# Performance work log

Measured on AMD Instinct MI355X. Metric: run time of the kernel, lower is better.

## Reference

```python
import jax, jax.numpy as jnp
import numpy as np

B, D, A = 512, 32, 18          # batch, n_latent_dims (= n_heads), n_actions
FED, AED = 128, 64             # factor/action embed dims
VD = FED + AED                 # vdim = 192
KD = VD                        # kdim (key_embed_dim=None -> vdim)
HID = 256                      # per-head MLP hidden size
H = D                          # n_heads = n_latent_dims


def setup_inputs() -> dict:
    key = jax.random.key(0)
    ks = jax.random.split(key, 20)
    s = lambda i, shape: jax.random.normal(ks[i], shape, dtype=jnp.float32) * 0.05
    return {
        "features": jax.random.normal(ks[0], (B, D), dtype=jnp.float32),
        "actions": jax.random.uniform(ks[1], (B, A), dtype=jnp.float32),
        # linear projections (stored as [in, out], i.e. torch weight.T)
        "Wq": s(2, (A, KD)),  "bq": s(3, (KD,)),      # action_query_projection
        "Wk": s(4, (D, KD)),  "bk": s(5, (KD,)),      # factor_key_projection
        "Wav": s(6, (A, AED)), "bav": s(7, (AED,)),   # action_val_projection
        "Wfv": s(8, (D, FED)), "bfv": s(9, (FED,)),   # factor_val_projection
        # per-head input MLPs: vdim -> HID -> vdim (ReLU)
        "W1": s(10, (H, VD, HID)), "b1": s(11, (H, HID)),
        "W2": s(12, (H, HID, VD)), "b2": s(13, (H, VD)),
        # per-head output MLPs: vdim -> HID -> 1 (ReLU)
        "W1o": s(14, (H, VD, HID)), "b1o": s(15, (H, HID)),
        "W2o": s(16, (H, HID)),     "b2o": s(17, (H,)),
    }


def reference(features, actions, Wq, bq, Wk, bk, Wav, bav, Wfv, bfv,
              W1, b1, W2, b2, W1o, b1o, W2o, b2o):
    z, a = features, actions
    # diag_embed(z) row i = z_i * e_i, so Linear(diag_embed(z))[..., i, :] = z_i * W.T[i] + b.
    # z is expanded identically across heads, so factor embeds/keys are head-independent.
    factor_embeds = z[:, :, None] * Wfv[None] + bfv          # [B, D, FED]
    keys = z[:, :, None] * Wk[None] + bk                     # [B, D, KD]
    queries = a @ Wq + bq                                    # [B, KD]
    action_embeds = a @ Wav + bav                            # [B, AED]

    # concat factor vals with broadcast action vals -> [B, D, VD]
    cv = jnp.concatenate(
        [factor_embeds, jnp.broadcast_to(action_embeds[:, None, :], (B, D, AED))], axis=-1)

    # per-head input MLPs (ReLU), batched over heads via einsum
    h = jax.nn.relu(jnp.einsum('bdv,hvk->bhdk', cv, W1) + b1[None, :, None, :])
    values = jnp.einsum('bhdk,hkv->bhdv', h, W2) + b2[None, :, None, :]  # [B,H,D,VD]

    # attention: single query vs D keys; head-independent weights
    scores = (keys @ queries[:, :, None])[..., 0] / jnp.sqrt(jnp.float32(KD))  # [B, D]
    w = jax.nn.softmax(scores, axis=-1)                       # [B, D]
    attn_out = jnp.einsum('bd,bhdv->bhv', w, values)          # [B, H, VD]

    # per-head output MLPs (ReLU) -> scalar effect per head
    h2 = jax.nn.relu(jnp.einsum('bhv,hvk->bhk', attn_out, W1o) + b1o[None])
    effect = jnp.einsum('bhk,hk->bh', h2, W2o) + b2o[None]    # [B, H]

    attn_weights = jnp.broadcast_to(w[:, None, :], (B, H, D))  # [B, H, D]
    return effect, attn_weights
```

## Files before the change

kernel.cpp:

```cpp
#include <hip/hip_runtime.h>
#include <hip/hip_bf16.h>


typedef __attribute__((ext_vector_type(8))) short bf16x8;
typedef __attribute__((ext_vector_type(4))) short bf16x4;
typedef __attribute__((ext_vector_type(4))) float f32x4;

__device__ __forceinline__ short f2bf(float x) {
  unsigned u = __float_as_uint(x);
  u += 0x7fffu + ((u >> 16) & 1u);
  return (short)(u >> 16);
}
__device__ __forceinline__ float bf2f(unsigned short u) {
  return __uint_as_float((unsigned)u << 16);
}

__global__ __launch_bounds__(256) void kA_prep(
    const float* __restrict__ feat, const float* __restrict__ act,
    const float* __restrict__ Wq, const float* __restrict__ bq,
    const float* __restrict__ Wk,
    const float* __restrict__ Wav, const float* __restrict__ bav,
    const float* __restrict__ Wfv, const float* __restrict__ bfv,
    const float* __restrict__ W1, const float* __restrict__ b1,
    const float* __restrict__ W2, const float* __restrict__ b2,
    const float* __restrict__ W1o, const float* __restrict__ b1o,
    float* __restrict__ ws_w, float* __restrict__ ws_U,
    float* __restrict__ ws_c0, unsigned short* __restrict__ ws_Mbf,
    float* __restrict__ ws_c1, float* __restrict__ ws_W1g,
    float* __restrict__ out_aw) {
  __shared__ __align__(16) char smem[33792];
  float* sh = (float*)smem;
  const int bx = blockIdx.x;
  const int t = threadIdx.x;

  if (bx < 64) {
    const int b0 = bx * 8;
    float* sWk = sh;
    float* sA  = sh + 6144;
    float* sQk = sh + 6320;
    float* sW  = sh + 6944;
#pragma unroll
    for (int i = 0; i < 24; ++i) {
      const int idx = i * 256 + t;
      sWk[(idx % 192) * 32 + (idx / 192)] = Wk[idx];
    }
    if (t < 144) sA[t] = act[b0 * 18 + t];
    __syncthreads();
    for (int o = t; o < 608; o += 256) {
      const int j = o >> 5, d = o & 31;
      const float* arow = (j < 18) ? (Wq + j * 192) : bq;
      float acc = 0.f;
      for (int c = 0; c < 192; ++c) acc += arow[c] * sWk[c * 32 + d];
      sQk[o] = acc;
    }
    __syncthreads();
    {
      const int bi = t >> 5, d = t & 31;
      float dot = sQk[18 * 32 + d];
#pragma unroll
      for (int j = 0; j < 18; ++j) dot += sA[bi * 18 + j] * sQk[j * 32 + d];
      const float z = feat[b0 * 32 + t];
      float sc = z * dot * 0.07216878364870322f;
      float mx = sc;
#pragma unroll
      for (int off = 16; off >= 1; off >>= 1) mx = fmaxf(mx, __shfl_xor(mx, off, 64));
      const float e = __expf(sc - mx);
      float s = e;
#pragma unroll
      for (int off = 16; off >= 1; off >>= 1) s += __shfl_xor(s, off, 64);
      const float w = e / s;
      ws_w[b0 * 32 + t] = w;
      sW[t] = w;
    }
    __syncthreads();
#pragma unroll
    for (int i = 0; i < 32; ++i)
      out_aw[b0 * 1024 + i * 256 + t] = sW[(i >> 2) * 32 + (t & 31)];

  } else if (bx < 224) {
    const int r = bx - 64;
    const int h = r / 5, dt = r % 5;
    float* sF = sh;
    if (dt < 4) {
#pragma unroll
      for (int i = 0; i < 4; ++i) sF[i * 256 + t] = Wfv[dt * 1024 + i * 256 + t];
    } else {
      if (t < 128) sF[t] = bfv[t];
    }
    __syncthreads();
    if (dt < 4) {
      float acc[8];
#pragma unroll
      for (int dd = 0; dd < 8; ++dd) acc[dd] = 0.f;
#pragma unroll 4
      for (int fc = 0; fc < 32; ++fc) {
        float w1v[4];
#pragma unroll
        for (int u = 0; u < 4; ++u) w1v[u] = W1[(h * 192 + fc * 4 + u) * 256 + t];
#pragma unroll
        for (int dd = 0; dd < 8; ++dd) {
          float4 f4 = *(const float4*)(sF + dd * 128 + fc * 4);
          acc[dd] += f4.x * w1v[0] + f4.y * w1v[1] + f4.z * w1v[2] + f4.w * w1v[3];
        }
      }
#pragma unroll
      for (int dd = 0; dd < 8; ++dd)
        ws_U[(h * 32 + dt * 8 + dd) * 256 + t] = acc[dd];
    } else {
      float acc = b1[h * 256 + t];
      for (int fc = 0; fc < 32; ++fc) {
        float w1v[4];
#pragma unroll
        for (int u = 0; u < 4; ++u) w1v[u] = W1[(h * 192 + fc * 4 + u) * 256 + t];
        float4 f4 = *(const float4*)(sF + fc * 4);
        acc += f4.x * w1v[0] + f4.y * w1v[1] + f4.z * w1v[2] + f4.w * w1v[3];
      }
      for (int u = 0; u < 64; ++u)
        acc += bav[u] * W1[(h * 192 + 128 + u) * 256 + t];
      ws_c0[h * 256 + t] = acc;
    }

  } else if (bx < 480) {
    const int r = bx - 224;
    const int h = r >> 3, kt = r & 7;
    short* sW2 = (short*)smem;
    short* sB  = (short*)(smem + 13184);

    for (int i = t; i < 6144; i += 256) {
      const int row = i / 192, col = i - row * 192;
      sW2[row * 206 + col] = f2bf(W2[h * 49152 + (kt * 32 + row) * 192 + col]);
    }
    const int wv = t >> 6, lane = t & 63;
    const int quad = lane >> 4, l15 = lane & 15;

    f32x4 acc[2][4];
    const f32x4 zero = {0.f, 0.f, 0.f, 0.f};
#pragma unroll
    for (int mt = 0; mt < 2; ++mt)
#pragma unroll
      for (int nt = 0; nt < 4; ++nt) acc[mt][nt] = zero;
    float c1acc = 0.f;

    for (int kk = 0; kk < 6; ++kk) {
      __syncthreads();
#pragma unroll
      for (int vp = 0; vp < 32; vp += 2) {
        const float f0 = W1o[h * 49152 + (kk * 32 + vp) * 256 + t];
        const float f1 = W1o[h * 49152 + (kk * 32 + vp + 1) * 256 + t];
        const unsigned pack =
            ((unsigned)(unsigned short)f2bf(f1) << 16) | (unsigned short)f2bf(f0);
        *(unsigned*)(sB + t * 38 + vp) = pack;
      }
      __syncthreads();
      if (kt == 0) {
#pragma unroll
        for (int vp = 0; vp < 32; ++vp)
          c1acc += b2[h * 192 + kk * 32 + vp] * bf2f((unsigned short)sB[t * 38 + vp]);
      }
      bf16x8 a0[2];
#pragma unroll
      for (int mt = 0; mt < 2; ++mt)
        a0[mt] = *(const bf16x8*)(sW2 + (mt * 16 + l15) * 206 + kk * 32 + quad * 8);
#pragma unroll
      for (int nt = 0; nt < 4; ++nt) {
        bf16x8 b0 = *(const bf16x8*)(sB + (wv * 64 + nt * 16 + l15) * 38 + quad * 8);
#pragma unroll
        for (int mt = 0; mt < 2; ++mt)
          acc[mt][nt] = __builtin_amdgcn_mfma_f32_16x16x32_bf16(a0[mt], b0, acc[mt][nt], 0, 0, 0);
      }
    }
#pragma unroll
    for (int mt = 0; mt < 2; ++mt) {
#pragma unroll
      for (int nt = 0; nt < 4; ++nt) {
        const int col = wv * 64 + nt * 16 + l15;
        const unsigned p0 = ((unsigned)(unsigned short)f2bf(acc[mt][nt][1]) << 16) |
                            (unsigned short)f2bf(acc[mt][nt][0]);
        const unsigned p1 = ((unsigned)(unsigned short)f2bf(acc[mt][nt][3]) << 16) |
                            (unsigned short)f2bf(acc[mt][nt][2]);
        unsigned* dst = (unsigned*)(ws_Mbf + (size_t)(h * 256 + col) * 256 +
                                    kt * 32 + mt * 16 + quad * 4);
        dst[0] = p0; dst[1] = p1;
      }
    }
    if (kt == 0) ws_c1[h * 256 + t] = c1acc + b1o[h * 256 + t];

  } else {
    const int h = bx - 480;
    float accj[18];
#pragma unroll
    for (int j = 0; j < 18; ++j) accj[j] = 0.f;
#pragma unroll 4
    for (int u = 0; u < 64; ++u) {
      const float w1v = W1[(h * 192 + 128 + u) * 256 + t];
#pragma unroll
      for (int j = 0; j < 18; ++j)
        accj[j] += Wav[j * 64 + u] * w1v;
    }
#pragma unroll
    for (int j = 0; j < 18; ++j)
      ws_W1g[(h * 20 + j) * 256 + t] = accj[j];
    ws_W1g[(h * 20 + 18) * 256 + t] = 0.f;
    ws_W1g[(h * 20 + 19) * 256 + t] = 0.f;
  }
}

__global__ __launch_bounds__(256) void kB_main(
    const float* __restrict__ feat, const float* __restrict__ act,
    const float* __restrict__ ws_w, const float* __restrict__ ws_U,
    const float* __restrict__ ws_W1g, const float* __restrict__ ws_c0,
    const unsigned short* __restrict__ ws_Mbf, const float* __restrict__ ws_c1,
    const float* __restrict__ W2o, const float* __restrict__ b2o,
    float* __restrict__ out_eff) {
  const int bx = blockIdx.x;
  const int h = (bx & 7) * 4 + ((bx >> 3) & 3);
  const int bt = bx >> 5;
  const int b0 = bt * 16;
  const int t = threadIdx.x;

  __shared__ __align__(16) char smem[14208];
  short* sP   = (short*)smem;
  float* sA   = (float*)(smem + 8448);
  float* sZ   = (float*)(smem + 9728);
  float* sWw  = (float*)(smem + 11776);
  float* sRed = (float*)(smem + 13824);

  {
#pragma unroll
    for (int i = 0; i < 2; ++i) {
      sZ[i * 256 + t]  = feat[b0 * 32 + i * 256 + t];
      sWw[i * 256 + t] = ws_w[b0 * 32 + i * 256 + t];
    }
    for (int i = t; i < 320; i += 256) {
      const int row = i / 20, col = i - row * 20;
      sA[i] = (col < 18) ? act[(b0 + row) * 18 + col] : 0.f;
    }
  }
  __syncthreads();

  {
    const int bq = t >> 6, kg = t & 63;
    float g[4][4];

    {
      float4 c04 = *(const float4*)(ws_c0 + h * 256 + kg * 4);
#pragma unroll
      for (int r = 0; r < 4; ++r) {
        g[r][0] = c04.x; g[r][1] = c04.y; g[r][2] = c04.z; g[r][3] = c04.w;
      }
      const float* Wgp = ws_W1g + (h * 20) * 256 + kg * 4;
#pragma unroll
      for (int jc = 0; jc < 5; ++jc) {
        float w1q[4][4];
#pragma unroll
        for (int u = 0; u < 4; ++u) {
          float4 w4 = *(const float4*)(Wgp + (jc * 4 + u) * 256);
          w1q[u][0] = w4.x; w1q[u][1] = w4.y; w1q[u][2] = w4.z; w1q[u][3] = w4.w;
        }
        float a4[4][4];
#pragma unroll
        for (int r = 0; r < 4; ++r) {
          float4 av = *(const float4*)(sA + (bq * 4 + r) * 20 + jc * 4);
          a4[r][0] = av.x; a4[r][1] = av.y; a4[r][2] = av.z; a4[r][3] = av.w;
        }
#pragma unroll
        for (int u = 0; u < 4; ++u)
#pragma unroll
          for (int r = 0; r < 4; ++r)
#pragma unroll
            for (int c = 0; c < 4; ++c)
              g[r][c] += a4[r][u] * w1q[u][c];
      }
    }

    float acc[4][4];
#pragma unroll
    for (int r = 0; r < 4; ++r) {
      acc[r][0] = 0.f; acc[r][1] = 0.f; acc[r][2] = 0.f; acc[r][3] = 0.f;
    }
    const float* Up = ws_U + h * 8192 + kg * 4;
#pragma unroll
    for (int dc = 0; dc < 8; ++dc) {
      float uc[4][4];
#pragma unroll
      for (int dd = 0; dd < 4; ++dd) {
        float4 u4 = *(const float4*)(Up + (dc * 4 + dd) * 256);
        uc[dd][0] = u4.x; uc[dd][1] = u4.y; uc[dd][2] = u4.z; uc[dd][3] = u4.w;
      }
      float zr[4][4], wr[4][4];
#pragma unroll
      for (int r = 0; r < 4; ++r) {
        float4 z4 = *(const float4*)(sZ + (bq * 4 + r) * 32 + dc * 4);
        float4 w4 = *(const float4*)(sWw + (bq * 4 + r) * 32 + dc * 4);
        zr[r][0] = z4.x; zr[r][1] = z4.y; zr[r][2] = z4.z; zr[r][3] = z4.w;
        wr[r][0] = w4.x; wr[r][1] = w4.y; wr[r][2] = w4.z; wr[r][3] = w4.w;
      }
#pragma unroll
      for (int dd = 0; dd < 4; ++dd) {
#pragma unroll
        for (int r = 0; r < 4; ++r) {
#pragma unroll
          for (int c = 0; c < 4; ++c)
            acc[r][c] += wr[r][dd] * fmaxf(zr[r][dd] * uc[dd][c] + g[r][c], 0.f);
        }
      }
    }
#pragma unroll
    for (int r = 0; r < 4; ++r) {
      bf16x4 p;
#pragma unroll
      for (int c = 0; c < 4; ++c) p[c] = f2bf(acc[r][c]);
      *(bf16x4*)(sP + (bq * 4 + r) * 264 + kg * 4) = p;
    }
  }
  __syncthreads();

  {
    const int wv = t >> 6;
    const int lane = t & 63;
    const int quad = lane >> 4, l15 = lane & 15;

    f32x4 acc[4];
    const f32x4 zero = {0.f, 0.f, 0.f, 0.f};
#pragma unroll
    for (int nt = 0; nt < 4; ++nt) acc[nt] = zero;

    float c1r[4], w2r[4];
#pragma unroll
    for (int nt = 0; nt < 4; ++nt) {
      const int col = wv * 64 + nt * 16 + l15;
      c1r[nt] = ws_c1[h * 256 + col];
      w2r[nt] = W2o[h * 256 + col];
    }
    const unsigned short* Mp = ws_Mbf + (size_t)(h * 256 + wv * 64) * 256;

#pragma unroll
    for (int kc = 0; kc < 8; ++kc) {
      bf16x8 a0 = *(const bf16x8*)(sP + l15 * 264 + kc * 32 + quad * 8);
      bf16x8 bfr[4];
#pragma unroll
      for (int nt = 0; nt < 4; ++nt)
        bfr[nt] = *(const bf16x8*)(Mp + (nt * 16 + l15) * 256 + kc * 32 + quad * 8);
#pragma unroll
      for (int nt = 0; nt < 4; ++nt)
        acc[nt] = __builtin_amdgcn_mfma_f32_16x16x32_bf16(a0, bfr[nt], acc[nt], 0, 0, 0);
    }
#pragma unroll
    for (int r = 0; r < 4; ++r) {
      float s = fmaxf(acc[0][r] + c1r[0], 0.f) * w2r[0]
              + fmaxf(acc[1][r] + c1r[1], 0.f) * w2r[1]
              + fmaxf(acc[2][r] + c1r[2], 0.f) * w2r[2]
              + fmaxf(acc[3][r] + c1r[3], 0.f) * w2r[3];
      s += __shfl_xor(s, 1, 64);
      s += __shfl_xor(s, 2, 64);
      s += __shfl_xor(s, 4, 64);
      s += __shfl_xor(s, 8, 64);
      if (l15 == 0) sRed[(quad * 4 + r) * 4 + wv] = s;
    }
  }
  __syncthreads();
  if (t < 16) {
    float v = sRed[t * 4] + sRed[t * 4 + 1] + sRed[t * 4 + 2] + sRed[t * 4 + 3] + b2o[h];
    out_eff[(b0 + t) * 32 + h] = v;
  }
}

extern "C" void kernel_launch(void* const* d_in, const int* in_sizes, int n_in,
                              void* d_out, int out_size, void* d_ws, size_t ws_size,
                              hipStream_t stream) {
  const float* feat = (const float*)d_in[0];
  const float* act  = (const float*)d_in[1];
  const float* Wq   = (const float*)d_in[2];
  const float* bq   = (const float*)d_in[3];
  const float* Wk   = (const float*)d_in[4];
  const float* Wav  = (const float*)d_in[6];
  const float* bav  = (const float*)d_in[7];
  const float* Wfv  = (const float*)d_in[8];
  const float* bfv  = (const float*)d_in[9];
  const float* W1   = (const float*)d_in[10];
  const float* b1   = (const float*)d_in[11];
  const float* W2   = (const float*)d_in[12];
  const float* b2   = (const float*)d_in[13];
  const float* W1o  = (const float*)d_in[14];
  const float* b1o  = (const float*)d_in[15];
  const float* W2o  = (const float*)d_in[16];
  const float* b2o  = (const float*)d_in[17];
  float* out = (float*)d_out;
  float* ws = (float*)d_ws;

  float* ws_w  = ws;
  float* ws_U  = ws + 16384;
  float* ws_c0 = ws + 278528;
  float* ws_c1 = ws + 286720;
  unsigned short* ws_Mbf = (unsigned short*)(ws + 294912);
  float* ws_W1g = ws + 1343488;

  hipLaunchKernelGGL(kA_prep, dim3(512), dim3(256), 0, stream,
                     feat, act, Wq, bq, Wk, Wav, bav, Wfv, bfv, W1, b1,
                     W2, b2, W1o, b1o, ws_w, ws_U, ws_c0, ws_Mbf, ws_c1,
                     ws_W1g, out + 16384);
  hipLaunchKernelGGL(kB_main, dim3(1024), dim3(256), 0, stream,
                     feat, act, ws_w, ws_U, ws_W1g, ws_c0, ws_Mbf, ws_c1,
                     W2o, b2o, out);
}
```

Before: 146.3 us.

## Process 32 batch rows per block in kB_main with 2x2 MFMA tiles

Doubles the batch tile per block in the main kernel from 16 to 32 rows and raises the block to 512 threads across 8 waves. Each wave now covers 32 output columns for two 16-row M tiles instead of 64 columns for one. This is meant to halve the number of times the per-head bf16 M matrix and the other per-head constants are read from global memory. In exchange it halves the grid to 512 blocks, which lowers the number of blocks in flight, and needs more shared memory per block.

```diff
diff --git a/kernel.cpp b/kernel.cpp
--- a/kernel.cpp
+++ b/kernel.cpp
@@ -205,7 +205,7 @@
   }
 }
 
-__global__ __launch_bounds__(256) void kB_main(
+__global__ __launch_bounds__(512) void kB_main(
     const float* __restrict__ feat, const float* __restrict__ act,
     const float* __restrict__ ws_w, const float* __restrict__ ws_U,
     const float* __restrict__ ws_W1g, const float* __restrict__ ws_c0,
@@ -215,23 +215,23 @@
   const int bx = blockIdx.x;
   const int h = (bx & 7) * 4 + ((bx >> 3) & 3);
   const int bt = bx >> 5;
-  const int b0 = bt * 16;
+  const int b0 = bt * 32;
   const int t = threadIdx.x;
 
-  __shared__ __align__(16) char smem[14208];
+  __shared__ __align__(16) char smem[28672];
   short* sP   = (short*)smem;
-  float* sA   = (float*)(smem + 8448);
-  float* sZ   = (float*)(smem + 9728);
-  float* sWw  = (float*)(smem + 11776);
-  float* sRed = (float*)(smem + 13824);
+  float* sA   = (float*)(smem + 16896);
+  float* sZ   = (float*)(smem + 19456);
+  float* sWw  = (float*)(smem + 23552);
+  float* sRed = (float*)(smem + 27648);
 
   {
 #pragma unroll
     for (int i = 0; i < 2; ++i) {
-      sZ[i * 256 + t]  = feat[b0 * 32 + i * 256 + t];
-      sWw[i * 256 + t] = ws_w[b0 * 32 + i * 256 + t];
-    }
-    for (int i = t; i < 320; i += 256) {
+      sZ[i * 512 + t]  = feat[b0 * 32 + i * 512 + t];
+      sWw[i * 512 + t] = ws_w[b0 * 32 + i * 512 + t];
+    }
+    for (int i = t; i < 640; i += 512) {
       const int row = i / 20, col = i - row * 20;
       sA[i] = (col < 18) ? act[(b0 + row) * 18 + col] : 0.f;
     }
@@ -320,47 +320,57 @@
     const int lane = t & 63;
     const int quad = lane >> 4, l15 = lane & 15;
 
-    f32x4 acc[4];
+    f32x4 acc[2][2];
     const f32x4 zero = {0.f, 0.f, 0.f, 0.f};
 #pragma unroll
-    for (int nt = 0; nt < 4; ++nt) acc[nt] = zero;
-
-    float c1r[4], w2r[4];
-#pragma unroll
-    for (int nt = 0; nt < 4; ++nt) {
-      const int col = wv * 64 + nt * 16 + l15;
+    for (int mt = 0; mt < 2; ++mt)
+#pragma unroll
+      for (int nt = 0; nt < 2; ++nt) acc[mt][nt] = zero;
+
+    float c1r[2], w2r[2];
+#pragma unroll
+    for (int nt = 0; nt < 2; ++nt) {
+      const int col = wv * 32 + nt * 16 + l15;
       c1r[nt] = ws_c1[h * 256 + col];
       w2r[nt] = W2o[h * 256 + col];
     }
-    const unsigned short* Mp = ws_Mbf + (size_t)(h * 256 + wv * 64) * 256;
+    const unsigned short* Mp = ws_Mbf + (size_t)(h * 256 + wv * 32) * 256;
 
 #pragma unroll
     for (int kc = 0; kc < 8; ++kc) {
-      bf16x8 a0 = *(const bf16x8*)(sP + l15 * 264 + kc * 32 + quad * 8);
-      bf16x8 bfr[4];
-#pragma unroll
-      for (int nt = 0; nt < 4; ++nt)
+      bf16x8 a0[2];
+#pragma unroll
+      for (int mt = 0; mt < 2; ++mt)
+        a0[mt] = *(const bf16x8*)(sP + (mt * 16 + l15) * 264 + kc * 32 + quad * 8);
+      bf16x8 bfr[2];
+#pragma unroll
+      for (int nt = 0; nt < 2; ++nt)
         bfr[nt] = *(const bf16x8*)(Mp + (nt * 16 + l15) * 256 + kc * 32 + quad * 8);
 #pragma unroll
-      for (int nt = 0; nt < 4; ++nt)
-        acc[nt] = __builtin_amdgcn_mfma_f32_16x16x32_bf16(a0, bfr[nt], acc[nt], 0, 0, 0);
-    }
-#pragma unroll
-    for (int r = 0; r < 4; ++r) {
-      float s = fmaxf(acc[0][r] + c1r[0], 0.f) * w2r[0]
-              + fmaxf(acc[1][r] + c1r[1], 0.f) * w2r[1]
-              + fmaxf(acc[2][r] + c1r[2], 0.f) * w2r[2]
-              + fmaxf(acc[3][r] + c1r[3], 0.f) * w2r[3];
-      s += __shfl_xor(s, 1, 64);
-      s += __shfl_xor(s, 2, 64);
-      s += __shfl_xor(s, 4, 64);
-      s += __shfl_xor(s, 8, 64);
-      if (l15 == 0) sRed[(quad * 4 + r) * 4 + wv] = s;
+      for (int nt = 0; nt < 2; ++nt)
+#pragma unroll
+        for (int mt = 0; mt < 2; ++mt)
+          acc[mt][nt] = __builtin_amdgcn_mfma_f32_16x16x32_bf16(a0[mt], bfr[nt], acc[mt][nt], 0, 0, 0);
+    }
+#pragma unroll
+    for (int mt = 0; mt < 2; ++mt) {
+#pragma unroll
+      for (int r = 0; r < 4; ++r) {
+        float s = fmaxf(acc[mt][0][r] + c1r[0], 0.f) * w2r[0]
+                + fmaxf(acc[mt][1][r] + c1r[1], 0.f) * w2r[1];
+        s += __shfl_xor(s, 1, 64);
+        s += __shfl_xor(s, 2, 64);
+        s += __shfl_xor(s, 4, 64);
+        s += __shfl_xor(s, 8, 64);
+        if (l15 == 0) sRed[(mt * 16 + quad * 4 + r) * 8 + wv] = s;
+      }
     }
   }
   __syncthreads();
-  if (t < 16) {
-    float v = sRed[t * 4] + sRed[t * 4 + 1] + sRed[t * 4 + 2] + sRed[t * 4 + 3] + b2o[h];
+  if (t < 32) {
+    float v = b2o[h];
+#pragma unroll
+    for (int wv = 0; wv < 8; ++wv) v += sRed[t * 8 + wv];
     out_eff[(b0 + t) * 32 + h] = v;
   }
 }
@@ -399,7 +409,7 @@
                      feat, act, Wq, bq, Wk, Wav, bav, Wfv, bfv, W1, b1,
                      W2, b2, W1o, b1o, ws_w, ws_U, ws_c0, ws_Mbf, ws_c1,
                      ws_W1g, out + 16384);
-  hipLaunchKernelGGL(kB_main, dim3(1024), dim3(256), 0, stream,
+  hipLaunchKernelGGL(kB_main, dim3(512), dim3(512), 0, stream,
                      feat, act, ws_w, ws_U, ws_W1g, ws_c0, ws_Mbf, ws_c1,
                      W2o, b2o, out);
 }
```

Result: no change. 146.9 us (+0.4%).
